# Kernel tuning notes

Measured on AMD Instinct MI355X. Metric: run time of the kernel, lower is better.

Reference implementation:

```python
import jax, jax.numpy as jnp
import numpy as np

D_STATE = 16
D_CONV = 4

def layernorm(x, g, b, eps=1e-5):
    m = jnp.mean(x, -1, keepdims=True)
    v = jnp.var(x, -1, keepdims=True)
    return (x - m) / jnp.sqrt(v + eps) * g + b

def conv1x1(x, w):  # x [b,h,w,cin], w [cin,cout]
    return jnp.einsum('bhwc,cd->bhwd', x, w)

def dwconv3x3(x, w):  # x [b,h,w,C], w [3,3,1,C] (HWIO, groups=C)
    return jax.lax.conv_general_dilated(x, w, (1, 1), 'SAME',
        dimension_numbers=('NHWC', 'HWIO', 'NHWC'),
        feature_group_count=x.shape[-1])

def causal_dwconv1d(x, w, b):  # x [B,L,D], w [K,1,D]; causal depthwise conv (Mamba d_conv=4)
    xp = jnp.pad(x, ((0, 0), (D_CONV - 1, 0), (0, 0)))
    y = jax.lax.conv_general_dilated(xp, w, (1,), 'VALID',
        dimension_numbers=('NWC', 'WIO', 'NWC'),
        feature_group_count=x.shape[-1])
    return y + b

def selective_scan(deltaA, deltaBx, C):
    # deltaA, deltaBx: [B,L,D,S]; C: [B,L,S] -> y: [B,L,D]
    def step(h, inp):
        dA, dBx, c = inp
        h = dA * h + dBx
        return h, jnp.einsum('bds,bs->bd', h, c)
    h0 = jnp.zeros(deltaA.shape[:1] + deltaA.shape[2:], deltaA.dtype)
    _, ys = jax.lax.scan(step, h0,
        (jnp.swapaxes(deltaA, 0, 1), jnp.swapaxes(deltaBx, 0, 1), jnp.swapaxes(C, 0, 1)))
    return jnp.swapaxes(ys, 0, 1)

def spa_ssm(x, in_w, conv_w, conv_b, xproj_w, dt_w, dt_b, Alog, D, out_w):
    # Mamba (slow path) applied to flattened spatial sequence; x: [b,h,w,c]
    b, h, w, c = x.shape
    L = h * w
    xs = x.reshape(b, L, c)
    di = Alog.shape[0]
    xz = xs @ in_w                       # [b,L,2*di]
    xi, z = xz[..., :di], xz[..., di:]
    xi = jax.nn.silu(causal_dwconv1d(xi, conv_w, conv_b))
    dbc = xi @ xproj_w                   # [b,L,dt_rank+2*S]
    dtr = dt_w.shape[0]
    dt = jax.nn.softplus(dbc[..., :dtr] @ dt_w + dt_b)   # [b,L,di]
    B = dbc[..., dtr:dtr + D_STATE]
    C = dbc[..., dtr + D_STATE:]
    A = -jnp.exp(Alog)                   # [di,S]
    deltaA = jnp.exp(dt[..., None] * A)                  # [b,L,di,S]
    deltaBx = (dt * xi)[..., None] * B[:, :, None, :]    # [b,L,di,S]
    y = selective_scan(deltaA, deltaBx, C) + D * xi
    y = y * jax.nn.silu(z)
    return (y @ out_w).reshape(b, h, w, c)

def camba_forward(x, ln1_g, ln1_b, vin_w1, vin_dw, vin_w2, vout_dw1, vout_dw2,
                  ssm_in_w, ssm_conv_w, ssm_conv_b, ssm_xproj_w, ssm_dt_w, ssm_dt_b,
                  ssm_Alog, ssm_D, ssm_out_w, ln2_g, ln2_b, ff_w1, ff_dw, ff_w2):
    x = jnp.transpose(x, (0, 2, 3, 1))   # [b,h,w,c]
    # ESSM: v_in_head = LN -> 1x1 -> dw3x3 -> GELU -> 1x1
    x0 = conv1x1(layernorm(x, ln1_g, ln1_b), vin_w1)
    x0 = jax.nn.gelu(dwconv3x3(x0, vin_dw), approximate=False)
    x0 = conv1x1(x0, vin_w2)
    y = spa_ssm(x0, ssm_in_w, ssm_conv_w, ssm_conv_b, ssm_xproj_w,
                ssm_dt_w, ssm_dt_b, ssm_Alog, ssm_D, ssm_out_w) + x0
    # v_out_head = dw3x3 -> GELU -> dw3x3, residual
    y = dwconv3x3(jax.nn.gelu(dwconv3x3(y, vout_dw1), approximate=False), vout_dw2) + y
    x = y + x                            # block residual
    # PreNorm FeedForward (mult=4): 1x1 -> LReLU -> dw3x3 -> LReLU -> 1x1
    t = layernorm(x, ln2_g, ln2_b)
    t = jax.nn.leaky_relu(conv1x1(t, ff_w1), 0.2)
    t = jax.nn.leaky_relu(dwconv3x3(t, ff_dw), 0.2)
    t = conv1x1(t, ff_w2)
    x = t + x
    return jnp.transpose(x, (0, 3, 1, 2))

def setup_inputs() -> dict:
    key = jax.random.key(0)
    ks = jax.random.split(key, 16)
    b, c, h, w = 8, 64, 64, 64
    di, ds, dtr = 128, 16, 4
    s = 0.05
    n = lambda k, shp: jax.random.normal(k, shp, jnp.float32) * s
    dt0 = jnp.exp(jax.random.uniform(ks[1], (di,)) * (np.log(0.1) - np.log(1e-3)) + np.log(1e-3))
    return dict(
        x=jax.random.normal(ks[0], (b, c, h, w), jnp.float32),
        ln1_g=jnp.ones(c), ln1_b=jnp.zeros(c),
        vin_w1=n(ks[2], (c, c)), vin_dw=n(ks[3], (3, 3, 1, c)), vin_w2=n(ks[4], (c, c)),
        vout_dw1=n(ks[5], (3, 3, 1, c)), vout_dw2=n(ks[6], (3, 3, 1, c)),
        ssm_in_w=n(ks[7], (c, 2 * di)),
        ssm_conv_w=n(ks[8], (D_CONV, 1, di)), ssm_conv_b=jnp.zeros(di),
        ssm_xproj_w=n(ks[9], (di, dtr + 2 * ds)),
        ssm_dt_w=n(ks[10], (dtr, di)), ssm_dt_b=jnp.log(jnp.expm1(dt0)),
        ssm_Alog=jnp.log(jnp.broadcast_to(jnp.arange(1., ds + 1), (di, ds))),
        ssm_D=jnp.ones(di),
        ssm_out_w=n(ks[11], (di, c)),
        ln2_g=jnp.ones(c), ln2_b=jnp.zeros(c),
        ff_w1=n(ks[12], (c, 4 * c)), ff_dw=n(ks[13], (3, 3, 1, 4 * c)), ff_w2=n(ks[14], (4 * c, c)),
    )

def reference(x, ln1_g, ln1_b, vin_w1, vin_dw, vin_w2, vout_dw1, vout_dw2,
              ssm_in_w, ssm_conv_w, ssm_conv_b, ssm_xproj_w, ssm_dt_w, ssm_dt_b,
              ssm_Alog, ssm_D, ssm_out_w, ln2_g, ln2_b, ff_w1, ff_dw, ff_w2):
    return camba_forward(x, ln1_g, ln1_b, vin_w1, vin_dw, vin_w2, vout_dw1, vout_dw2,
                         ssm_in_w, ssm_conv_w, ssm_conv_b, ssm_xproj_w, ssm_dt_w, ssm_dt_b,
                         ssm_Alog, ssm_D, ssm_out_w, ln2_g, ln2_b, ff_w1, ff_dw, ff_w2)
```

## Files before the change

kernel.cpp:

```cpp
#include <hip/hip_runtime.h>
#include <hip/hip_bf16.h>
#include <math.h>

typedef unsigned short u16;
typedef __attribute__((ext_vector_type(8))) short s8v;
typedef __attribute__((ext_vector_type(4))) float f4v;

#define B_    8
#define C_    64
#define HW_   4096
#define NPIX  32768
#define DI    128
#define NCH   256
#define CHL   16

__device__ __forceinline__ float b2f(u16 v){ return __uint_as_float(((unsigned)v)<<16); }
__device__ __forceinline__ u16 f2b(float x){
  unsigned u = __float_as_uint(x);
  u += 0x7fff + ((u >> 16) & 1);
  return (u16)(u >> 16);
}
__device__ __forceinline__ float gelu_exact(float x){ return 0.5f*x*(1.0f+erff(x*0.70710678118654752f)); }
__device__ __forceinline__ float leaky02(float x){ return x>0.f ? x : 0.2f*x; }
__device__ __forceinline__ float softplus_(float x){ return fmaxf(x,0.f)+log1pf(__expf(-fabsf(x))); }
__device__ __forceinline__ float silu_(float x){ return x / (1.0f + __expf(-x)); }
__device__ __forceinline__ void unpack16(uint4 q0, uint4 q1, float* v){
  unsigned w[8]={q0.x,q0.y,q0.z,q0.w,q1.x,q1.y,q1.z,q1.w};
  #pragma unroll
  for(int j=0;j<8;j++){
    v[2*j]   = __uint_as_float(w[j]<<16);
    v[2*j+1] = __uint_as_float(w[j]&0xffff0000u);
  }
}

__global__ void k_prep(const float* __restrict__ vin_w1, const float* __restrict__ vin_w2,
                       const float* __restrict__ ssm_in_w, const float* __restrict__ xproj,
                       const float* __restrict__ dtw, const float* __restrict__ ssm_outw,
                       const float* __restrict__ ff_w1, const float* __restrict__ ff_w2,
                       u16* __restrict__ wv1, u16* __restrict__ wv2, u16* __restrict__ wsi,
                       u16* __restrict__ wdb, u16* __restrict__ wout, u16* __restrict__ wf1,
                       u16* __restrict__ wf2t){
  int g = blockIdx.x*256 + threadIdx.x;
  if(g < 4096){
    int n=g>>6, c=g&63;
    wv1[n*64+c]=f2b(vin_w1[c*64+n]);
    wv2[n*64+c]=f2b(vin_w2[c*64+n]);
  }
  if(g < 16384){
    int n=g>>6, c=g&63;
    wsi[n*64+c]=f2b(ssm_in_w[c*256+n]);
    wf1[n*64+c]=f2b(ff_w1[c*256+n]);
    int n2=g/256, k2=g%256;
    wf2t[n2*256+k2]=f2b(ff_w2[k2*64+n2]);
  }
  if(g < 8192){
    int n=g>>7, k=g&127;
    wout[n*128+k]=f2b(ssm_outw[k*64+n]);
  }
  if(g < 20480){
    int n=g/128, k=g%128;
    float v;
    if(n < 128){
      v = 0.f;
      for(int r=0;r<4;r++) v += xproj[k*36+r]*dtw[r*128+n];
    }else{
      v = xproj[k*36+4+(n-128)];
    }
    wdb[n*128+k]=f2b(v);
  }
}

__global__ __launch_bounds__(256) void k_trans_ln_mm(const float* __restrict__ x,
                     const float* __restrict__ g, const float* __restrict__ bta,
                     const u16* __restrict__ wT,
                     u16* __restrict__ xT, u16* __restrict__ outp){
  const int LDA = 72, NS = 4;
  __shared__ float tile[64][65];
  __shared__ __align__(16) u16 sA[64*LDA];
  __shared__ __align__(16) u16 sW[64*LDA];
  int tid = threadIdx.x;
  int blk = blockIdx.x;
  int b = blk >> 6;
  int hwb = (blk & 63) << 6;
  int lane = tid & 63, row = tid >> 6;
  const float* src = x + (size_t)b*C_*HW_;
  #pragma unroll
  for(int k=0;k<16;k++){
    int c = row + 4*k;
    tile[c][lane] = src[c*HW_ + hwb + lane];
  }
  for(int idx=tid; idx<64*8; idx+=256){
    int n = idx>>3, c8 = (idx&7)*8;
    *(uint4*)(sW + n*LDA + c8) = *(const uint4*)(wT + n*64 + c8);
  }
  __syncthreads();
  u16* dstT = xT + (size_t)b*HW_*C_;
  #pragma unroll
  for(int k=0;k<16;k++){
    int hwl = row + 4*k;
    dstT[(hwb+hwl)*C_ + lane] = f2b(tile[lane][hwl]);
  }
  float gg = g[lane], bb = bta[lane];
  #pragma unroll
  for(int i=0;i<16;i++){
    int hwl = row*16 + i;
    float v = tile[lane][hwl];
    float s = v, sq = v*v;
    #pragma unroll
    for(int o=32;o>0;o>>=1){ s += __shfl_xor(s,o); sq += __shfl_xor(sq,o); }
    float m = s*(1.f/64.f);
    float var = sq*(1.f/64.f) - m*m;
    float r = rsqrtf(var + 1e-5f);
    sA[hwl*LDA + lane] = f2b((v-m)*r*gg + bb);
  }
  __syncthreads();
  int ln = tid & 63, wv = tid >> 6;
  int mrow = ln & 15, quad = ln >> 4;
  f4v acc[NS];
  #pragma unroll
  for(int i=0;i<NS;i++) acc[i] = (f4v){0.f,0.f,0.f,0.f};
  const u16* aBase = sA + (wv*16 + mrow)*LDA + quad*8;
  const u16* wBase = sW + mrow*LDA + quad*8;
  #pragma unroll
  for(int kk=0; kk<64; kk+=32){
    s8v af = *(const s8v*)(aBase + kk);
    #pragma unroll
    for(int ns=0; ns<NS; ns++){
      s8v bf = *(const s8v*)(wBase + ns*16*LDA + kk);
      acc[ns] = __builtin_amdgcn_mfma_f32_16x16x32_bf16(af, bf, acc[ns], 0, 0, 0);
    }
  }
  int p0 = blk*64;
  int pr = p0 + wv*16 + quad*4;
  #pragma unroll
  for(int ns=0; ns<NS; ns++){
    int n = ns*16 + mrow;
    #pragma unroll
    for(int r=0;r<4;r++)
      outp[(size_t)(pr+r)*64 + n] = f2b(acc[ns][r]);
  }
}

__global__ __launch_bounds__(256) void k_dw3mm(const u16* __restrict__ in,
                     const float* __restrict__ dwgt, const u16* __restrict__ wT,
                     u16* __restrict__ x0){
  const int LDT = 72;
  __shared__ __align__(16) u16 sIn[10*10*64];
  __shared__ __align__(16) u16 sT[64*LDT];
  __shared__ __align__(16) u16 sW[64*LDT];
  int tid = threadIdx.x;
  int blk = blockIdx.x;
  int b = blk >> 6;
  int t6 = blk & 63;
  int h0 = (t6 >> 3) * 8, w0 = (t6 & 7) * 8;
  for(int idx=tid; idx<64*8; idx+=256){
    int n = idx>>3, c8 = (idx&7)*8;
    *(uint4*)(sW + n*LDT + c8) = *(const uint4*)(wT + n*64 + c8);
  }
  for(int q=tid; q<10*10*16; q+=256){
    int pp = q >> 4, c4 = q & 15;
    int hh = pp / 10, ww = pp % 10;
    int gh = h0-1+hh, gw = w0-1+ww;
    ushort4 v = make_ushort4(0,0,0,0);
    if((unsigned)gh < 64u && (unsigned)gw < 64u)
      v = *(const ushort4*)(in + (size_t)((b*64+gh)*64+gw)*64 + c4*4);
    *(ushort4*)(sIn + pp*64 + c4*4) = v;
  }
  __syncthreads();
  int c4 = tid & 15;
  #pragma unroll
  for(int pass=0; pass<4; pass++){
    int opix = pass*16 + (tid>>4);
    int oh = opix >> 3, ow = opix & 7;
    float a0=0.f,a1=0.f,a2=0.f,a3=0.f;
    #pragma unroll
    for(int kh=0;kh<3;kh++){
      #pragma unroll
      for(int kw=0;kw<3;kw++){
        ushort4 v = *(const ushort4*)(sIn + ((oh+kh)*10 + (ow+kw))*64 + c4*4);
        float4 wv = *(const float4*)(dwgt + (kh*3+kw)*64 + c4*4);
        a0 += b2f(v.x)*wv.x; a1 += b2f(v.y)*wv.y;
        a2 += b2f(v.z)*wv.z; a3 += b2f(v.w)*wv.w;
      }
    }
    ushort4 o; o.x=f2b(gelu_exact(a0)); o.y=f2b(gelu_exact(a1));
    o.z=f2b(gelu_exact(a2)); o.w=f2b(gelu_exact(a3));
    *(ushort4*)(sT + opix*LDT + c4*4) = o;
  }
  __syncthreads();
  int ln = tid & 63, wv = tid >> 6;
  int mrow = ln & 15, quad = ln >> 4;
  f4v acc[4];
  #pragma unroll
  for(int i=0;i<4;i++) acc[i] = (f4v){0.f,0.f,0.f,0.f};
  const u16* aBase = sT + (wv*16 + mrow)*LDT + quad*8;
  const u16* wBase = sW + mrow*LDT + quad*8;
  #pragma unroll
  for(int kk=0; kk<64; kk+=32){
    s8v af = *(const s8v*)(aBase + kk);
    #pragma unroll
    for(int ns=0; ns<4; ns++){
      s8v bf = *(const s8v*)(wBase + ns*16*LDT + kk);
      acc[ns] = __builtin_amdgcn_mfma_f32_16x16x32_bf16(af, bf, acc[ns], 0, 0, 0);
    }
  }
  #pragma unroll
  for(int ns=0; ns<4; ns++){
    int n = ns*16 + mrow;
    #pragma unroll
    for(int r=0;r<4;r++){
      int opix = wv*16 + quad*4 + r;
      int oh = opix >> 3, ow = opix & 7;
      size_t p = ((size_t)(b*64 + h0+oh)*64 + (w0+ow));
      x0[p*64 + n] = f2b(acc[ns][r]);
    }
  }
}

__global__ __launch_bounds__(256) void k_ssm_dtbc(const u16* __restrict__ wT,
                     const u16* __restrict__ x0,
                     const float* __restrict__ cw, const float* __restrict__ cb,
                     const u16* __restrict__ wdb, const float* __restrict__ dtbias,
                     u16* __restrict__ xi, u16* __restrict__ zs,
                     u16* __restrict__ dtout, u16* __restrict__ bcout){
  const int LDA=72, NS=16, LDY=136, LDWD=136, NS2=10;
  __shared__ __align__(16) u16 S[31616];
  u16* sW   = S;
  u16* sA   = S + 18432;
  u16* ubuf = S + 23040;
  u16* xiT  = S;
  u16* wdbS = S + 8704;
  int tid = threadIdx.x;
  int p0 = blockIdx.x*64;
  int ln = tid & 63, wv = tid >> 6;
  int mrow = ln & 15, quad = ln >> 4;
  for(int idx=tid; idx<256*8; idx+=256){
    int n = idx>>3, c8 = (idx&7)*8;
    *(uint4*)(sW + n*LDA + c8) = *(const uint4*)(wT + n*64 + c8);
  }
  for(int g=tid; g<64*8; g+=256){
    int row = g >> 3, c8 = (g & 7)*8;
    *(uint4*)(sA + row*LDA + c8) = *(const uint4*)(x0 + (size_t)(p0+row)*64 + c8);
  }
  __syncthreads();
  f4v acc[NS];
  #pragma unroll
  for(int i=0;i<NS;i++) acc[i] = (f4v){0.f,0.f,0.f,0.f};
  const u16* aBase = sA + (wv*16 + mrow)*LDA + quad*8;
  const u16* wBase = sW + mrow*LDA + quad*8;
  #pragma unroll
  for(int kk=0; kk<64; kk+=32){
    s8v af = *(const s8v*)(aBase + kk);
    #pragma unroll
    for(int ns=0; ns<NS; ns++){
      s8v bf = *(const s8v*)(wBase + ns*16*LDA + kk);
      acc[ns] = __builtin_amdgcn_mfma_f32_16x16x32_bf16(af, bf, acc[ns], 0, 0, 0);
    }
  }
  bool bstart = ((p0 & 4095) == 0);
  for(int idx=tid; idx<384; idx+=256){
    int j = idx >> 7, n = idx & 127;
    float a2 = 0.f;
    if(!bstart){
      const u16* xr = x0 + (size_t)(p0-3+j)*64;
      #pragma unroll 8
      for(int c=0;c<64;c++) a2 += b2f(xr[c]) * b2f(sW[n*LDA+c]);
    }
    ubuf[j*128 + n] = f2b(a2);
  }
  int prl = wv*16 + quad*4;
  #pragma unroll
  for(int ns=0; ns<NS; ns++){
    int n = ns*16 + mrow;
    if(n < 128){
      #pragma unroll
      for(int r=0;r<4;r++) ubuf[(prl+r+3)*128 + n] = f2b(acc[ns][r]);
    }else{
      #pragma unroll
      for(int r=0;r<4;r++) zs[(size_t)(p0+prl+r)*128 + (n-128)] = f2b(silu_(acc[ns][r]));
    }
  }
  __syncthreads();
  int d4 = tid & 31;
  float4 cbv = *(const float4*)(cb + d4*4);
  for(int row = tid >> 5; row < 64; row += 8){
    float a0=cbv.x, a1=cbv.y, a2=cbv.z, a3=cbv.w;
    #pragma unroll
    for(int k=0;k<4;k++){
      ushort4 v = *(const ushort4*)(ubuf + (row+k)*128 + d4*4);
      float4 wv4 = *(const float4*)(cw + k*128 + d4*4);
      a0 += b2f(v.x)*wv4.x; a1 += b2f(v.y)*wv4.y;
      a2 += b2f(v.z)*wv4.z; a3 += b2f(v.w)*wv4.w;
    }
    ushort4 o; o.x=f2b(silu_(a0)); o.y=f2b(silu_(a1)); o.z=f2b(silu_(a2)); o.w=f2b(silu_(a3));
    *(ushort4*)(xi + (size_t)(p0+row)*128 + d4*4) = o;
    *(ushort4*)(xiT + row*LDY + d4*4) = o;
  }
  __syncthreads();
  for(int idx=tid; idx<160*16; idx+=256){
    int n = idx>>4, c8 = (idx&15)*8;
    *(uint4*)(wdbS + n*LDWD + c8) = *(const uint4*)(wdb + n*128 + c8);
  }
  __syncthreads();
  f4v acc2[NS2];
  #pragma unroll
  for(int i=0;i<NS2;i++) acc2[i] = (f4v){0.f,0.f,0.f,0.f};
  #pragma unroll
  for(int kk=0; kk<128; kk+=32){
    s8v af = *(const s8v*)(xiT + (wv*16+mrow)*LDY + kk + quad*8);
    #pragma unroll
    for(int ns=0; ns<NS2; ns++){
      s8v bf = *(const s8v*)(wdbS + (ns*16+mrow)*LDWD + kk + quad*8);
      acc2[ns] = __builtin_amdgcn_mfma_f32_16x16x32_bf16(af, bf, acc2[ns], 0, 0, 0);
    }
  }
  int pr = p0 + wv*16 + quad*4;
  #pragma unroll
  for(int ns=0; ns<NS2; ns++){
    int n = ns*16 + mrow;
    if(n < 128){
      float bs = dtbias[n];
      #pragma unroll
      for(int r=0;r<4;r++)
        dtout[(size_t)(pr+r)*128 + n] = f2b(softplus_(acc2[ns][r] + bs));
    }else{
      #pragma unroll
      for(int r=0;r<4;r++)
        bcout[(size_t)(pr+r)*32 + (n-128)] = f2b(acc2[ns][r]);
    }
  }
}

__global__ __launch_bounds__(256) void k_scan1(const u16* __restrict__ dt, const u16* __restrict__ xi,
                        const u16* __restrict__ bc, const float* __restrict__ alog,
                        u16* __restrict__ Pb, u16* __restrict__ Qb){
  int t = blockIdx.x*256 + threadIdx.x;
  int d = t & 127;
  int ch = (t >> 7) & 255;
  int b = t >> 15;
  int pbase = b*HW_ + ch*CHL;
  float A[16];
  #pragma unroll
  for(int s=0;s<16;s++) A[s] = -__expf(alog[d*16+s]);
  float dtv[16], uv[16];
  #pragma unroll
  for(int i=0;i<CHL;i++){
    dtv[i] = b2f(dt[(size_t)(pbase+i)*128 + d]);
    uv[i]  = dtv[i] * b2f(xi[(size_t)(pbase+i)*128 + d]);
  }
  float Q[16], sumdt = 0.f;
  #pragma unroll
  for(int s=0;s<16;s++) Q[s] = 0.f;
  #pragma unroll
  for(int i=0;i<CHL;i++){
    float Bv[16];
    unpack16(*(const uint4*)(bc + (size_t)(pbase+i)*32),
             *(const uint4*)(bc + (size_t)(pbase+i)*32 + 8), Bv);
    sumdt += dtv[i];
    #pragma unroll
    for(int s=0;s<16;s++){
      float a = __expf(dtv[i]*A[s]);
      Q[s] = a*Q[s] + uv[i]*Bv[s];
    }
  }
  int gidx = ch*16384 + (b*128+d)*16;
  unsigned pw[8], qw[8];
  #pragma unroll
  for(int j=0;j<8;j++){
    pw[j] = (unsigned)f2b(__expf(A[2*j]*sumdt)) | ((unsigned)f2b(__expf(A[2*j+1]*sumdt))<<16);
    qw[j] = (unsigned)f2b(Q[2*j]) | ((unsigned)f2b(Q[2*j+1])<<16);
  }
  *(uint4*)(Pb+gidx)   = make_uint4(pw[0],pw[1],pw[2],pw[3]);
  *(uint4*)(Pb+gidx+8) = make_uint4(pw[4],pw[5],pw[6],pw[7]);
  *(uint4*)(Qb+gidx)   = make_uint4(qw[0],qw[1],qw[2],qw[3]);
  *(uint4*)(Qb+gidx+8) = make_uint4(qw[4],qw[5],qw[6],qw[7]);
}

__global__ __launch_bounds__(256) void k_scan2(const u16* __restrict__ Pb, const u16* __restrict__ Qb,
                        u16* __restrict__ Hin){
  __shared__ __align__(16) u16 sP[256*32];
  __shared__ __align__(16) u16 sQ[256*32];
  __shared__ float gP[8*32];
  __shared__ float gQ[8*32];
  int tid = threadIdx.x;
  int s0 = blockIdx.x * 32;
  for(int idx = tid; idx < 256*4; idx += 256){
    int ch = idx >> 2, j8 = (idx & 3) * 8;
    *(uint4*)(sP + ch*32 + j8) = *(const uint4*)(Pb + (size_t)ch*16384 + s0 + j8);
    *(uint4*)(sQ + ch*32 + j8) = *(const uint4*)(Qb + (size_t)ch*16384 + s0 + j8);
  }
  __syncthreads();
  int sl = tid & 31, grp = tid >> 5;
  int base = grp * 32;
  float P = 1.f, Q = 0.f;
  #pragma unroll 8
  for(int c = 0; c < 32; c++){
    float p = b2f(sP[(base+c)*32 + sl]);
    float q = b2f(sQ[(base+c)*32 + sl]);
    P = p * P;
    Q = p * Q + q;
  }
  gP[grp*32 + sl] = P;
  gQ[grp*32 + sl] = Q;
  __syncthreads();
  float h = 0.f;
  #pragma unroll
  for(int g = 0; g < 7; g++){
    if(g < grp) h = gP[g*32 + sl] * h + gQ[g*32 + sl];
  }
  for(int c = 0; c < 32; c++){
    Hin[(size_t)(base+c)*16384 + s0 + sl] = f2b(h);
    float p = b2f(sP[(base+c)*32 + sl]);
    float q = b2f(sQ[(base+c)*32 + sl]);
    h = p * h + q;
  }
}

__global__ __launch_bounds__(128) void k_scan3_mm(const u16* __restrict__ dt, const u16* __restrict__ xi,
                        const u16* __restrict__ bc, const u16* __restrict__ zs,
                        const float* __restrict__ alog, const float* __restrict__ Dp,
                        const u16* __restrict__ Hin, const u16* __restrict__ wout,
                        const u16* __restrict__ x0, u16* __restrict__ y){
  const int LDY = 136, LDW = 136;
  int blk = blockIdx.x;
  int ch = blk & (NCH-1);
  int b = blk >> 8;
  int d = threadIdx.x, tid = threadIdx.x;
  __shared__ __align__(16) u16 sY[CHL*LDY];
  __shared__ __align__(16) u16 sWo[64*LDW];
  __shared__ __align__(16) u16 sbc[CHL*32];
  for(int idx=tid; idx<64*16; idx+=128){
    int n = idx>>4, c8 = (idx&15)*8;
    *(uint4*)(sWo + n*LDW + c8) = *(const uint4*)(wout + n*128 + c8);
  }
  int pbase = b*HW_ + ch*CHL;
  if(tid < 64) ((uint4*)sbc)[tid] = ((const uint4*)(bc + (size_t)pbase*32))[tid];
  float A[16], h[16];
  u16 hbuf[16];
  int gidx = ch*16384 + (b*128+d)*16;
  *(uint4*)hbuf     = *(const uint4*)(Hin+gidx);
  *(uint4*)(hbuf+8) = *(const uint4*)(Hin+gidx+8);
  #pragma unroll
  for(int s=0;s<16;s++){ A[s] = -__expf(alog[d*16+s]); h[s] = b2f(hbuf[s]); }
  float Dd = Dp[d];
  float dtv[16], xiv[16], zsv[16];
  #pragma unroll
  for(int i=0;i<CHL;i++){
    dtv[i] = b2f(dt[(size_t)(pbase+i)*128 + d]);
    xiv[i] = b2f(xi[(size_t)(pbase+i)*128 + d]);
    zsv[i] = b2f(zs[(size_t)(pbase+i)*128 + d]);
  }
  __syncthreads();
  #pragma unroll
  for(int i=0;i<CHL;i++){
    float Bv[16], Cv[16];
    unpack16(*(const uint4*)(sbc + i*32),      *(const uint4*)(sbc + i*32 + 8),  Bv);
    unpack16(*(const uint4*)(sbc + i*32 + 16), *(const uint4*)(sbc + i*32 + 24), Cv);
    float u = dtv[i]*xiv[i];
    float acc = Dd*xiv[i];
    #pragma unroll
    for(int s=0;s<16;s++){
      float a = __expf(dtv[i]*A[s]);
      h[s] = a*h[s] + u*Bv[s];
      acc += h[s]*Cv[s];
    }
    sY[i*LDY + d] = f2b(acc * zsv[i]);
  }
  __syncthreads();
  int ln = tid & 63, wv = tid >> 6;
  int mrow = ln & 15, quad = ln >> 4;
  f4v acc2[2];
  acc2[0] = (f4v){0.f,0.f,0.f,0.f};
  acc2[1] = (f4v){0.f,0.f,0.f,0.f};
  #pragma unroll
  for(int kk=0; kk<128; kk+=32){
    s8v af = *(const s8v*)(sY + mrow*LDY + kk + quad*8);
    #pragma unroll
    for(int ns=0; ns<2; ns++){
      int n0 = wv*32 + ns*16;
      s8v bf = *(const s8v*)(sWo + (n0+mrow)*LDW + kk + quad*8);
      acc2[ns] = __builtin_amdgcn_mfma_f32_16x16x32_bf16(af, bf, acc2[ns], 0, 0, 0);
    }
  }
  #pragma unroll
  for(int ns=0; ns<2; ns++){
    int n = wv*32 + ns*16 + mrow;
    #pragma unroll
    for(int r=0;r<4;r++){
      int px = pbase + quad*4 + r;
      y[(size_t)px*64 + n] = f2b(acc2[ns][r] + b2f(x0[(size_t)px*64 + n]));
    }
  }
}

__global__ __launch_bounds__(256) void k_ffn2(const u16* __restrict__ yin,
                     const float* __restrict__ w1, const float* __restrict__ w2,
                     const u16* __restrict__ xTr,
                     const float* __restrict__ g, const float* __restrict__ bta,
                     const u16* __restrict__ wf1, const u16* __restrict__ wf2t,
                     const float* __restrict__ fdw, float* __restrict__ outp){
  const int LDX = 72;
  extern __shared__ __align__(16) u16 S[];
  u16* sX  = S;
  u16* sC  = S + 8064;
  u16* sYh = S + 12672;
  u16* sT  = S + 26784;
  u16* sT1 = S + 12672;
  u16* sW1 = S + 20736;
  u16* sW2 = S + 25344;
  float* sDW = (float*)(S + 29952);
  int tid = threadIdx.x;
  int blk = blockIdx.x;
  int b = blk >> 6;
  int t6 = blk & 63;
  int h0 = (t6 >> 3)*8, w0 = (t6 & 7)*8;
  int ln = tid & 63, wv = tid >> 6;
  int mrow = ln & 15, quad = ln >> 4;
  for(int q=tid; q<196*16; q+=256){
    int pp = q >> 4, c4 = q & 15;
    int hh = pp / 14, ww = pp - hh*14;
    int gh = h0-3+hh, gw = w0-3+ww;
    ushort4 v = make_ushort4(0,0,0,0);
    if((unsigned)gh < 64u && (unsigned)gw < 64u)
      v = *(const ushort4*)(yin + (size_t)((b*64+gh)*64+gw)*64 + c4*4);
    *(ushort4*)(sYh + pp*LDX + c4*4) = v;
  }
  __syncthreads();
  for(int q=tid; q<144*16; q+=256){
    int tpix = q >> 4, c4 = q & 15;
    int th = tpix / 12, tw = tpix - th*12;
    int gh = h0-2+th, gw = w0-2+tw;
    ushort4 o = make_ushort4(0,0,0,0);
    if((unsigned)gh < 64u && (unsigned)gw < 64u){
      float a0=0.f,a1=0.f,a2=0.f,a3=0.f;
      #pragma unroll
      for(int kh=0;kh<3;kh++){
        #pragma unroll
        for(int kw=0;kw<3;kw++){
          ushort4 v = *(const ushort4*)(sYh + ((th+kh)*14 + (tw+kw))*LDX + c4*4);
          float4 wv4 = *(const float4*)(w1 + (kh*3+kw)*64 + c4*4);
          a0 += b2f(v.x)*wv4.x; a1 += b2f(v.y)*wv4.y;
          a2 += b2f(v.z)*wv4.z; a3 += b2f(v.w)*wv4.w;
        }
      }
      o.x=f2b(gelu_exact(a0)); o.y=f2b(gelu_exact(a1));
      o.z=f2b(gelu_exact(a2)); o.w=f2b(gelu_exact(a3));
    }
    *(ushort4*)(sT + tpix*LDX + c4*4) = o;
  }
  __syncthreads();
  for(int q=tid; q<100*16; q+=256){
    int xpix = q >> 4, c4 = q & 15;
    int xh = xpix / 10, xw = xpix - xh*10;
    int gh = h0-1+xh, gw = w0-1+xw;
    ushort4 o = make_ushort4(0,0,0,0);
    if((unsigned)gh < 64u && (unsigned)gw < 64u){
      float a0=0.f,a1=0.f,a2=0.f,a3=0.f;
      #pragma unroll
      for(int kh=0;kh<3;kh++){
        #pragma unroll
        for(int kw=0;kw<3;kw++){
          ushort4 v = *(const ushort4*)(sT + ((xh+kh)*12 + (xw+kw))*LDX + c4*4);
          float4 wv4 = *(const float4*)(w2 + (kh*3+kw)*64 + c4*4);
          a0 += b2f(v.x)*wv4.x; a1 += b2f(v.y)*wv4.y;
          a2 += b2f(v.z)*wv4.z; a3 += b2f(v.w)*wv4.w;
        }
      }
      ushort4 ry = *(const ushort4*)(sYh + ((xh+2)*14 + (xw+2))*LDX + c4*4);
      ushort4 rx = *(const ushort4*)(xTr + (size_t)((b*64+gh)*64+gw)*64 + c4*4);
      a0 += b2f(ry.x) + b2f(rx.x);
      a1 += b2f(ry.y) + b2f(rx.y);
      a2 += b2f(ry.z) + b2f(rx.z);
      a3 += b2f(ry.w) + b2f(rx.w);
      o.x=f2b(a0); o.y=f2b(a1); o.z=f2b(a2); o.w=f2b(a3);
    }
    *(ushort4*)(sX + xpix*LDX + c4*4) = o;
    if(xh>=1 && xh<=8 && xw>=1 && xw<=8)
      *(ushort4*)(sC + ((xh-1)*8 + (xw-1))*LDX + c4*4) = o;
  }
  __syncthreads();
  for(int i=tid; i<9*64; i+=256) ((float4*)sDW)[i] = ((const float4*)fdw)[i];
  float gg = g[ln], bb = bta[ln];
  for(int hp = wv; hp < 112; hp += 4){
    u16 o = 0;
    if(hp < 100){
      int th = hp/10, tw = hp - th*10;
      int gh = h0-1+th, gw = w0-1+tw;
      if((unsigned)gh < 64u && (unsigned)gw < 64u){
        float v = b2f(sX[hp*LDX + ln]);
        float s = v, sq = v*v;
        #pragma unroll
        for(int o2=32;o2>0;o2>>=1){ s += __shfl_xor(s,o2); sq += __shfl_xor(sq,o2); }
        float m = s*(1.f/64.f);
        float var = sq*(1.f/64.f) - m*m;
        float r = rsqrtf(var + 1e-5f);
        o = f2b((v-m)*r*gg + bb);
      }
    }
    sX[hp*LDX + ln] = o;
  }
  f4v acc2[4];
  #pragma unroll
  for(int i=0;i<4;i++) acc2[i] = (f4v){0.f,0.f,0.f,0.f};
  int p = wv*16 + mrow;
  int oh = p >> 3, ow = p & 7;
  for(int c=0; c<4; c++){
    int nc0 = c*64;
    __syncthreads();
    for(int idx=tid; idx<64*8; idx+=256){
      int n = idx>>3, c8 = (idx&7)*8;
      *(uint4*)(sW1 + n*LDX + c8) = *(const uint4*)(wf1 + (size_t)(nc0+n)*64 + c8);
      *(uint4*)(sW2 + n*LDX + c8) = *(const uint4*)(wf2t + (size_t)n*256 + nc0 + c8);
    }
    __syncthreads();
    for(int mt = wv; mt < 7; mt += 4){
      f4v a1[4];
      #pragma unroll
      for(int i=0;i<4;i++) a1[i] = (f4v){0.f,0.f,0.f,0.f};
      const u16* aB = sX + (mt*16 + mrow)*LDX + quad*8;
      const u16* wB = sW1 + mrow*LDX + quad*8;
      #pragma unroll
      for(int kk=0; kk<64; kk+=32){
        s8v af = *(const s8v*)(aB + kk);
        #pragma unroll
        for(int ns=0; ns<4; ns++){
          s8v bf = *(const s8v*)(wB + ns*16*LDX + kk);
          a1[ns] = __builtin_amdgcn_mfma_f32_16x16x32_bf16(af, bf, a1[ns], 0, 0, 0);
        }
      }
      #pragma unroll
      for(int ns=0; ns<4; ns++)
        #pragma unroll
        for(int r=0; r<4; r++)
          sT1[(mt*16 + quad*4 + r)*LDX + ns*16 + mrow] = f2b(leaky02(a1[ns][r]));
    }
    __syncthreads();
    #pragma unroll
    for(int half=0; half<2; half++){
      int ch0 = half*32 + quad*8;
      float a[8];
      #pragma unroll
      for(int j=0;j<8;j++) a[j] = 0.f;
      #pragma unroll
      for(int kh=0;kh<3;kh++){
        #pragma unroll
        for(int kw=0;kw<3;kw++){
          s8v v = *(const s8v*)(sT1 + ((oh+kh)*10 + (ow+kw))*LDX + ch0);
          const float* wp = sDW + (kh*3+kw)*256 + nc0 + ch0;
          float4 w0v = *(const float4*)(wp);
          float4 w1v = *(const float4*)(wp+4);
          a[0] += b2f((u16)v[0])*w0v.x; a[1] += b2f((u16)v[1])*w0v.y;
          a[2] += b2f((u16)v[2])*w0v.z; a[3] += b2f((u16)v[3])*w0v.w;
          a[4] += b2f((u16)v[4])*w1v.x; a[5] += b2f((u16)v[5])*w1v.y;
          a[6] += b2f((u16)v[6])*w1v.z; a[7] += b2f((u16)v[7])*w1v.w;
        }
      }
      s8v af;
      #pragma unroll
      for(int j=0;j<8;j++) af[j] = (short)f2b(leaky02(a[j]));
      #pragma unroll
      for(int ns=0; ns<4; ns++){
        s8v bf = *(const s8v*)(sW2 + (ns*16 + mrow)*LDX + half*32 + quad*8);
        acc2[ns] = __builtin_amdgcn_mfma_f32_16x16x32_bf16(af, bf, acc2[ns], 0, 0, 0);
      }
    }
  }
  int pe = wv*16 + quad*4;
  int eoh = pe >> 3, eow0 = pe & 7;
  #pragma unroll
  for(int ns=0; ns<4; ns++){
    int n = ns*16 + mrow;
    float4 v4;
    v4.x = acc2[ns][0] + b2f(sC[(pe+0)*LDX + n]);
    v4.y = acc2[ns][1] + b2f(sC[(pe+1)*LDX + n]);
    v4.z = acc2[ns][2] + b2f(sC[(pe+2)*LDX + n]);
    v4.w = acc2[ns][3] + b2f(sC[(pe+3)*LDX + n]);
    *(float4*)(outp + (size_t)b*C_*HW_ + (size_t)n*HW_ + (h0+eoh)*64 + (w0+eow0)) = v4;
  }
}

extern "C" void kernel_launch(void* const* d_in, const int* in_sizes, int n_in,
                              void* d_out, int out_size, void* d_ws, size_t ws_size,
                              hipStream_t stream) {
  const float* x        = (const float*)d_in[0];
  const float* ln1_g    = (const float*)d_in[1];
  const float* ln1_b    = (const float*)d_in[2];
  const float* vin_w1   = (const float*)d_in[3];
  const float* vin_dw   = (const float*)d_in[4];
  const float* vin_w2   = (const float*)d_in[5];
  const float* vout_dw1 = (const float*)d_in[6];
  const float* vout_dw2 = (const float*)d_in[7];
  const float* ssm_in_w = (const float*)d_in[8];
  const float* ssm_cw   = (const float*)d_in[9];
  const float* ssm_cb   = (const float*)d_in[10];
  const float* ssm_xprj = (const float*)d_in[11];
  const float* ssm_dtw  = (const float*)d_in[12];
  const float* ssm_dtb  = (const float*)d_in[13];
  const float* ssm_Alog = (const float*)d_in[14];
  const float* ssm_D    = (const float*)d_in[15];
  const float* ssm_outw = (const float*)d_in[16];
  const float* ln2_g    = (const float*)d_in[17];
  const float* ln2_b    = (const float*)d_in[18];
  const float* ff_w1    = (const float*)d_in[19];
  const float* ff_dw    = (const float*)d_in[20];
  const float* ff_w2    = (const float*)d_in[21];
  float* out = (float*)d_out;

  const size_t M = 1u<<20;
  u16* U   = (u16*)d_ws;
  u16* xT  = U;
  u16* tA  = U + 2*M;
  u16* tB  = U + 4*M;
  u16* x0  = U + 6*M;
  u16* xi  = U + 8*M;
  u16* zs  = U + 12*M;
  u16* dtb = U + 24*M;
  u16* bc  = U + 28*M;
  u16* Pb  = U + 16*M;
  u16* Qb  = U + 20*M;
  u16* Hin = tA;
  u16* y   = U + 16*M;
  u16* wv1  = U + 33*M;
  u16* wv2  = wv1 + 4096;
  u16* wsi  = wv2 + 4096;
  u16* wdb  = wsi + 16384;
  u16* wout = wdb + 20480;
  u16* wf1  = wout + 8192;
  u16* wf2t = wf1 + 16384;

  static bool attr_set = false;
  if(!attr_set){
    hipFuncSetAttribute((const void*)k_ffn2,
                        hipFuncAttributeMaxDynamicSharedMemorySize, 74304);
    attr_set = true;
  }

  k_prep<<<80,256,0,stream>>>(vin_w1, vin_w2, ssm_in_w, ssm_xprj, ssm_dtw, ssm_outw,
                              ff_w1, ff_w2, wv1, wv2, wsi, wdb, wout, wf1, wf2t);

  k_trans_ln_mm<<<512,256,0,stream>>>(x, ln1_g, ln1_b, wv1, xT, tB);
  k_dw3mm<<<512,256,0,stream>>>(tB, vin_dw, wv2, x0);

  k_ssm_dtbc<<<512,256,0,stream>>>(wsi, x0, ssm_cw, ssm_cb, wdb, ssm_dtb,
                                   xi, zs, dtb, bc);
  k_scan1<<<1024,256,0,stream>>>(dtb, xi, bc, ssm_Alog, Pb, Qb);
  k_scan2<<<512,256,0,stream>>>(Pb, Qb, Hin);
  k_scan3_mm<<<2048,128,0,stream>>>(dtb, xi, bc, zs, ssm_Alog, ssm_D, Hin, wout, x0, y);

  k_ffn2<<<512,256,74304,stream>>>(y, vout_dw1, vout_dw2, xT, ln2_g, ln2_b,
                                   wf1, wf2t, ff_dw, out);
}
```

Baseline: 246.0 us.

## Cut k_ffn2 shared memory by reading halo and weights from global

k_ffn2 no longer stages the 14x14 input halo, the FFN weight tiles or the depthwise weights in LDS. The first depthwise conv, the residual, and the MFMA B operands now read directly from global memory (expected to hit cache), and the per-chunk weight staging barriers are removed. LDS use falls from about 74KB of dynamic memory to about 46KB static, and launch_bounds(256,2) is added to k_ffn2 and k_ssm_dtbc so more blocks can be resident. The cost is more global/cache traffic and less coalesced B-operand loads inside the MFMA loops.

```diff
diff --git a/kernel.cpp b/kernel.cpp
--- a/kernel.cpp
+++ b/kernel.cpp
@@ -217,7 +217,7 @@
   }
 }
 
-__global__ __launch_bounds__(256) void k_ssm_dtbc(const u16* __restrict__ wT,
+__global__ __launch_bounds__(256, 2) void k_ssm_dtbc(const u16* __restrict__ wT,
                      const u16* __restrict__ x0,
                      const float* __restrict__ cw, const float* __restrict__ cb,
                      const u16* __restrict__ wdb, const float* __restrict__ dtbias,
@@ -493,22 +493,17 @@
   }
 }
 
-__global__ __launch_bounds__(256) void k_ffn2(const u16* __restrict__ yin,
+__global__ __launch_bounds__(256, 2) void k_ffn2(const u16* __restrict__ yin,
                      const float* __restrict__ w1, const float* __restrict__ w2,
                      const u16* __restrict__ xTr,
                      const float* __restrict__ g, const float* __restrict__ bta,
                      const u16* __restrict__ wf1, const u16* __restrict__ wf2t,
                      const float* __restrict__ fdw, float* __restrict__ outp){
   const int LDX = 72;
-  extern __shared__ __align__(16) u16 S[];
-  u16* sX  = S;
-  u16* sC  = S + 8064;
-  u16* sYh = S + 12672;
-  u16* sT  = S + 26784;
-  u16* sT1 = S + 12672;
-  u16* sW1 = S + 20736;
-  u16* sW2 = S + 25344;
-  float* sDW = (float*)(S + 29952);
+  __shared__ __align__(16) u16 sX[112*LDX];
+  __shared__ __align__(16) u16 sC[64*LDX];
+  __shared__ __align__(16) u16 sT[144*LDX];
+  u16* sT1 = sT;
   int tid = threadIdx.x;
   int blk = blockIdx.x;
   int b = blk >> 6;
@@ -516,16 +511,7 @@
   int h0 = (t6 >> 3)*8, w0 = (t6 & 7)*8;
   int ln = tid & 63, wv = tid >> 6;
   int mrow = ln & 15, quad = ln >> 4;
-  for(int q=tid; q<196*16; q+=256){
-    int pp = q >> 4, c4 = q & 15;
-    int hh = pp / 14, ww = pp - hh*14;
-    int gh = h0-3+hh, gw = w0-3+ww;
-    ushort4 v = make_ushort4(0,0,0,0);
-    if((unsigned)gh < 64u && (unsigned)gw < 64u)
-      v = *(const ushort4*)(yin + (size_t)((b*64+gh)*64+gw)*64 + c4*4);
-    *(ushort4*)(sYh + pp*LDX + c4*4) = v;
-  }
-  __syncthreads();
+  const u16* yb = yin + (size_t)b*HW_*64;
   for(int q=tid; q<144*16; q+=256){
     int tpix = q >> 4, c4 = q & 15;
     int th = tpix / 12, tw = tpix - th*12;
@@ -535,12 +521,18 @@
       float a0=0.f,a1=0.f,a2=0.f,a3=0.f;
       #pragma unroll
       for(int kh=0;kh<3;kh++){
-        #pragma unroll
-        for(int kw=0;kw<3;kw++){
-          ushort4 v = *(const ushort4*)(sYh + ((th+kh)*14 + (tw+kw))*LDX + c4*4);
-          float4 wv4 = *(const float4*)(w1 + (kh*3+kw)*64 + c4*4);
-          a0 += b2f(v.x)*wv4.x; a1 += b2f(v.y)*wv4.y;
-          a2 += b2f(v.z)*wv4.z; a3 += b2f(v.w)*wv4.w;
+        int hh = gh+kh-1;
+        if((unsigned)hh < 64u){
+          #pragma unroll
+          for(int kw=0;kw<3;kw++){
+            int ww = gw+kw-1;
+            if((unsigned)ww < 64u){
+              ushort4 v = *(const ushort4*)(yb + (size_t)(hh*64+ww)*64 + c4*4);
+              float4 wv4 = *(const float4*)(w1 + (kh*3+kw)*64 + c4*4);
+              a0 += b2f(v.x)*wv4.x; a1 += b2f(v.y)*wv4.y;
+              a2 += b2f(v.z)*wv4.z; a3 += b2f(v.w)*wv4.w;
+            }
+          }
         }
       }
       o.x=f2b(gelu_exact(a0)); o.y=f2b(gelu_exact(a1));
@@ -566,8 +558,8 @@
           a2 += b2f(v.z)*wv4.z; a3 += b2f(v.w)*wv4.w;
         }
       }
-      ushort4 ry = *(const ushort4*)(sYh + ((xh+2)*14 + (xw+2))*LDX + c4*4);
-      ushort4 rx = *(const ushort4*)(xTr + (size_t)((b*64+gh)*64+gw)*64 + c4*4);
+      ushort4 ry = *(const ushort4*)(yb + (size_t)(gh*64+gw)*64 + c4*4);
+      ushort4 rx = *(const ushort4*)(xTr + ((size_t)(b*64+gh)*64+gw)*64 + c4*4);
       a0 += b2f(ry.x) + b2f(rx.x);
       a1 += b2f(ry.y) + b2f(rx.y);
       a2 += b2f(ry.z) + b2f(rx.z);
@@ -579,7 +571,6 @@
       *(ushort4*)(sC + ((xh-1)*8 + (xw-1))*LDX + c4*4) = o;
   }
   __syncthreads();
-  for(int i=tid; i<9*64; i+=256) ((float4*)sDW)[i] = ((const float4*)fdw)[i];
   float gg = g[ln], bb = bta[ln];
   for(int hp = wv; hp < 112; hp += 4){
     u16 o = 0;
@@ -607,24 +598,17 @@
   for(int c=0; c<4; c++){
     int nc0 = c*64;
     __syncthreads();
-    for(int idx=tid; idx<64*8; idx+=256){
-      int n = idx>>3, c8 = (idx&7)*8;
-      *(uint4*)(sW1 + n*LDX + c8) = *(const uint4*)(wf1 + (size_t)(nc0+n)*64 + c8);
-      *(uint4*)(sW2 + n*LDX + c8) = *(const uint4*)(wf2t + (size_t)n*256 + nc0 + c8);
-    }
-    __syncthreads();
     for(int mt = wv; mt < 7; mt += 4){
       f4v a1[4];
       #pragma unroll
       for(int i=0;i<4;i++) a1[i] = (f4v){0.f,0.f,0.f,0.f};
       const u16* aB = sX + (mt*16 + mrow)*LDX + quad*8;
-      const u16* wB = sW1 + mrow*LDX + quad*8;
       #pragma unroll
       for(int kk=0; kk<64; kk+=32){
         s8v af = *(const s8v*)(aB + kk);
         #pragma unroll
         for(int ns=0; ns<4; ns++){
-          s8v bf = *(const s8v*)(wB + ns*16*LDX + kk);
+          s8v bf = *(const s8v*)(wf1 + (size_t)(nc0 + ns*16 + mrow)*64 + kk + quad*8);
           a1[ns] = __builtin_amdgcn_mfma_f32_16x16x32_bf16(af, bf, a1[ns], 0, 0, 0);
         }
       }
@@ -646,7 +630,7 @@
         #pragma unroll
         for(int kw=0;kw<3;kw++){
           s8v v = *(const s8v*)(sT1 + ((oh+kh)*10 + (ow+kw))*LDX + ch0);
-          const float* wp = sDW + (kh*3+kw)*256 + nc0 + ch0;
+          const float* wp = fdw + (kh*3+kw)*256 + nc0 + ch0;
           float4 w0v = *(const float4*)(wp);
           float4 w1v = *(const float4*)(wp+4);
           a[0] += b2f((u16)v[0])*w0v.x; a[1] += b2f((u16)v[1])*w0v.y;
@@ -660,7 +644,7 @@
       for(int j=0;j<8;j++) af[j] = (short)f2b(leaky02(a[j]));
       #pragma unroll
       for(int ns=0; ns<4; ns++){
-        s8v bf = *(const s8v*)(sW2 + (ns*16 + mrow)*LDX + half*32 + quad*8);
+        s8v bf = *(const s8v*)(wf2t + (size_t)(ns*16 + mrow)*256 + nc0 + half*32 + quad*8);
         acc2[ns] = __builtin_amdgcn_mfma_f32_16x16x32_bf16(af, bf, acc2[ns], 0, 0, 0);
       }
     }
@@ -728,13 +712,6 @@
   u16* wf1  = wout + 8192;
   u16* wf2t = wf1 + 16384;
 
-  static bool attr_set = false;
-  if(!attr_set){
-    hipFuncSetAttribute((const void*)k_ffn2,
-                        hipFuncAttributeMaxDynamicSharedMemorySize, 74304);
-    attr_set = true;
-  }
-
   k_prep<<<80,256,0,stream>>>(vin_w1, vin_w2, ssm_in_w, ssm_xprj, ssm_dtw, ssm_outw,
                               ff_w1, ff_w2, wv1, wv2, wsi, wdb, wout, wf1, wf2t);
 
@@ -747,6 +724,6 @@
   k_scan2<<<512,256,0,stream>>>(Pb, Qb, Hin);
   k_scan3_mm<<<2048,128,0,stream>>>(dtb, xi, bc, zs, ssm_Alog, ssm_D, Hin, wout, x0, y);
 
-  k_ffn2<<<512,256,74304,stream>>>(y, vout_dw1, vout_dw2, xT, ln2_g, ln2_b,
-                                   wf1, wf2t, ff_dw, out);
-}
+  k_ffn2<<<512,256,0,stream>>>(y, vout_dw1, vout_dw2, xT, ln2_g, ln2_b,
+                               wf1, wf2t, ff_dw, out);
+}
```

Result: slower. 262.6 us (+6.7%).

## Double ffn2 block to 512 threads, split K across wave groups, read weights from global

Applied to the files above, without the earlier changes.

The fused FFN kernel now runs 512 threads per block. The second 1x1 matmul's K dimension is split between two wave groups, and their partial sums are reduced through shared memory before the final store. The FFN weights and depthwise weights are no longer staged in LDS; they are read directly from global memory, which removes one barrier per chunk. Launch-bound occupancy hints are also added to k_ssm_dtbc. The aim is more latency hiding in the dominant kernel, at the cost of an extra reduction step and uncached global weight reads inside the inner loops.

```diff
diff --git a/kernel.cpp b/kernel.cpp
--- a/kernel.cpp
+++ b/kernel.cpp
@@ -217,7 +217,7 @@
   }
 }
 
-__global__ __launch_bounds__(256) void k_ssm_dtbc(const u16* __restrict__ wT,
+__global__ __launch_bounds__(256, 2) void k_ssm_dtbc(const u16* __restrict__ wT,
                      const u16* __restrict__ x0,
                      const float* __restrict__ cw, const float* __restrict__ cb,
                      const u16* __restrict__ wdb, const float* __restrict__ dtbias,
@@ -493,7 +493,7 @@
   }
 }
 
-__global__ __launch_bounds__(256) void k_ffn2(const u16* __restrict__ yin,
+__global__ __launch_bounds__(512, 4) void k_ffn2(const u16* __restrict__ yin,
                      const float* __restrict__ w1, const float* __restrict__ w2,
                      const u16* __restrict__ xTr,
                      const float* __restrict__ g, const float* __restrict__ bta,
@@ -506,9 +506,7 @@
   u16* sYh = S + 12672;
   u16* sT  = S + 26784;
   u16* sT1 = S + 12672;
-  u16* sW1 = S + 20736;
-  u16* sW2 = S + 25344;
-  float* sDW = (float*)(S + 29952);
+  float* red = (float*)(S + 26784);
   int tid = threadIdx.x;
   int blk = blockIdx.x;
   int b = blk >> 6;
@@ -516,7 +514,7 @@
   int h0 = (t6 >> 3)*8, w0 = (t6 & 7)*8;
   int ln = tid & 63, wv = tid >> 6;
   int mrow = ln & 15, quad = ln >> 4;
-  for(int q=tid; q<196*16; q+=256){
+  for(int q=tid; q<196*16; q+=512){
     int pp = q >> 4, c4 = q & 15;
     int hh = pp / 14, ww = pp - hh*14;
     int gh = h0-3+hh, gw = w0-3+ww;
@@ -526,7 +524,7 @@
     *(ushort4*)(sYh + pp*LDX + c4*4) = v;
   }
   __syncthreads();
-  for(int q=tid; q<144*16; q+=256){
+  for(int q=tid; q<144*16; q+=512){
     int tpix = q >> 4, c4 = q & 15;
     int th = tpix / 12, tw = tpix - th*12;
     int gh = h0-2+th, gw = w0-2+tw;
@@ -549,7 +547,7 @@
     *(ushort4*)(sT + tpix*LDX + c4*4) = o;
   }
   __syncthreads();
-  for(int q=tid; q<100*16; q+=256){
+  for(int q=tid; q<100*16; q+=512){
     int xpix = q >> 4, c4 = q & 15;
     int xh = xpix / 10, xw = xpix - xh*10;
     int gh = h0-1+xh, gw = w0-1+xw;
@@ -567,7 +565,7 @@
         }
       }
       ushort4 ry = *(const ushort4*)(sYh + ((xh+2)*14 + (xw+2))*LDX + c4*4);
-      ushort4 rx = *(const ushort4*)(xTr + (size_t)((b*64+gh)*64+gw)*64 + c4*4);
+      ushort4 rx = *(const ushort4*)(xTr + ((size_t)(b*64+gh)*64+gw)*64 + c4*4);
       a0 += b2f(ry.x) + b2f(rx.x);
       a1 += b2f(ry.y) + b2f(rx.y);
       a2 += b2f(ry.z) + b2f(rx.z);
@@ -579,9 +577,8 @@
       *(ushort4*)(sC + ((xh-1)*8 + (xw-1))*LDX + c4*4) = o;
   }
   __syncthreads();
-  for(int i=tid; i<9*64; i+=256) ((float4*)sDW)[i] = ((const float4*)fdw)[i];
   float gg = g[ln], bb = bta[ln];
-  for(int hp = wv; hp < 112; hp += 4){
+  for(int hp = wv; hp < 112; hp += 8){
     u16 o = 0;
     if(hp < 100){
       int th = hp/10, tw = hp - th*10;
@@ -602,29 +599,25 @@
   f4v acc2[4];
   #pragma unroll
   for(int i=0;i<4;i++) acc2[i] = (f4v){0.f,0.f,0.f,0.f};
-  int p = wv*16 + mrow;
-  int oh = p >> 3, ow = p & 7;
+  int grp = wv >> 2;
+  int pw = (wv & 3)*16 + mrow;
+  int oh = pw >> 3, ow = pw & 7;
+  int ch0 = grp*32 + quad*8;
   for(int c=0; c<4; c++){
     int nc0 = c*64;
     __syncthreads();
-    for(int idx=tid; idx<64*8; idx+=256){
-      int n = idx>>3, c8 = (idx&7)*8;
-      *(uint4*)(sW1 + n*LDX + c8) = *(const uint4*)(wf1 + (size_t)(nc0+n)*64 + c8);
-      *(uint4*)(sW2 + n*LDX + c8) = *(const uint4*)(wf2t + (size_t)n*256 + nc0 + c8);
-    }
-    __syncthreads();
-    for(int mt = wv; mt < 7; mt += 4){
+    if(wv < 7){
+      int mt = wv;
       f4v a1[4];
       #pragma unroll
       for(int i=0;i<4;i++) a1[i] = (f4v){0.f,0.f,0.f,0.f};
       const u16* aB = sX + (mt*16 + mrow)*LDX + quad*8;
-      const u16* wB = sW1 + mrow*LDX + quad*8;
       #pragma unroll
       for(int kk=0; kk<64; kk+=32){
         s8v af = *(const s8v*)(aB + kk);
         #pragma unroll
         for(int ns=0; ns<4; ns++){
-          s8v bf = *(const s8v*)(wB + ns*16*LDX + kk);
+          s8v bf = *(const s8v*)(wf1 + (size_t)(nc0 + ns*16 + mrow)*64 + kk + quad*8);
           a1[ns] = __builtin_amdgcn_mfma_f32_16x16x32_bf16(af, bf, a1[ns], 0, 0, 0);
         }
       }
@@ -635,9 +628,7 @@
           sT1[(mt*16 + quad*4 + r)*LDX + ns*16 + mrow] = f2b(leaky02(a1[ns][r]));
     }
     __syncthreads();
-    #pragma unroll
-    for(int half=0; half<2; half++){
-      int ch0 = half*32 + quad*8;
+    {
       float a[8];
       #pragma unroll
       for(int j=0;j<8;j++) a[j] = 0.f;
@@ -646,7 +637,7 @@
         #pragma unroll
         for(int kw=0;kw<3;kw++){
           s8v v = *(const s8v*)(sT1 + ((oh+kh)*10 + (ow+kw))*LDX + ch0);
-          const float* wp = sDW + (kh*3+kw)*256 + nc0 + ch0;
+          const float* wp = fdw + (kh*3+kw)*256 + nc0 + ch0;
           float4 w0v = *(const float4*)(wp);
           float4 w1v = *(const float4*)(wp+4);
           a[0] += b2f((u16)v[0])*w0v.x; a[1] += b2f((u16)v[1])*w0v.y;
@@ -660,22 +651,33 @@
       for(int j=0;j<8;j++) af[j] = (short)f2b(leaky02(a[j]));
       #pragma unroll
       for(int ns=0; ns<4; ns++){
-        s8v bf = *(const s8v*)(sW2 + (ns*16 + mrow)*LDX + half*32 + quad*8);
+        s8v bf = *(const s8v*)(wf2t + (size_t)(ns*16 + mrow)*256 + nc0 + ch0);
         acc2[ns] = __builtin_amdgcn_mfma_f32_16x16x32_bf16(af, bf, acc2[ns], 0, 0, 0);
       }
     }
   }
-  int pe = wv*16 + quad*4;
-  int eoh = pe >> 3, eow0 = pe & 7;
-  #pragma unroll
-  for(int ns=0; ns<4; ns++){
-    int n = ns*16 + mrow;
-    float4 v4;
-    v4.x = acc2[ns][0] + b2f(sC[(pe+0)*LDX + n]);
-    v4.y = acc2[ns][1] + b2f(sC[(pe+1)*LDX + n]);
-    v4.z = acc2[ns][2] + b2f(sC[(pe+2)*LDX + n]);
-    v4.w = acc2[ns][3] + b2f(sC[(pe+3)*LDX + n]);
-    *(float4*)(outp + (size_t)b*C_*HW_ + (size_t)n*HW_ + (h0+eoh)*64 + (w0+eow0)) = v4;
+  int pe = (wv & 3)*16 + quad*4;
+  if(grp == 1){
+    #pragma unroll
+    for(int ns=0; ns<4; ns++){
+      int n = ns*16 + mrow;
+      #pragma unroll
+      for(int r=0;r<4;r++) red[(pe+r)*64 + n] = acc2[ns][r];
+    }
+  }
+  __syncthreads();
+  if(grp == 0){
+    int eoh = pe >> 3, eow0 = pe & 7;
+    #pragma unroll
+    for(int ns=0; ns<4; ns++){
+      int n = ns*16 + mrow;
+      float4 v4;
+      v4.x = acc2[ns][0] + red[(pe+0)*64 + n] + b2f(sC[(pe+0)*LDX + n]);
+      v4.y = acc2[ns][1] + red[(pe+1)*64 + n] + b2f(sC[(pe+1)*LDX + n]);
+      v4.z = acc2[ns][2] + red[(pe+2)*64 + n] + b2f(sC[(pe+2)*LDX + n]);
+      v4.w = acc2[ns][3] + red[(pe+3)*64 + n] + b2f(sC[(pe+3)*LDX + n]);
+      *(float4*)(outp + (size_t)b*C_*HW_ + (size_t)n*HW_ + (h0+eoh)*64 + (w0+eow0)) = v4;
+    }
   }
 }
 
@@ -747,6 +749,6 @@
   k_scan2<<<512,256,0,stream>>>(Pb, Qb, Hin);
   k_scan3_mm<<<2048,128,0,stream>>>(dtb, xi, bc, zs, ssm_Alog, ssm_D, Hin, wout, x0, y);
 
-  k_ffn2<<<512,256,74304,stream>>>(y, vout_dw1, vout_dw2, xT, ln2_g, ln2_b,
+  k_ffn2<<<512,512,74304,stream>>>(y, vout_dw1, vout_dw2, xT, ln2_g, ln2_b,
                                    wf1, wf2t, ff_dw, out);
 }
```

After: 250.2 us. No clear change (+1.7%).
